# Optimization experiments

Measured on AMD Instinct MI355X. Metric: run time of the kernel, lower is better.

Reference implementation:

```python
import jax, jax.numpy as jnp
import numpy as np

B, S, C = 4, 4096, 1024
H, D, K = 16, 64, 256  # nhead, head_dim, dim_k


def setup_inputs() -> dict:
    key = jax.random.key(0)
    ks = jax.random.split(key, 7)
    x = jax.random.normal(ks[0], (B, S, C), dtype=jnp.float32)
    # per-head QKV projection weights (torch Linear weight layout [out,in])
    Wq = jax.random.normal(ks[1], (H, D, C), dtype=jnp.float32) * (C ** -0.5)
    Wk = jax.random.normal(ks[2], (H, D, C), dtype=jnp.float32) * (C ** -0.5)
    Wv = jax.random.normal(ks[3], (H, D, C), dtype=jnp.float32) * (C ** -0.5)
    # Linformer E/F sequence projections, per head: [K, S]
    We = jax.random.normal(ks[4], (H, K, S), dtype=jnp.float32) * (S ** -0.5)
    Wf = jax.random.normal(ks[5], (H, K, S), dtype=jnp.float32) * (S ** -0.5)
    # output projection (with bias, as w_o is nn.Linear default bias=True)
    Wo = jax.random.normal(ks[6], (C, H * D), dtype=jnp.float32) * ((H * D) ** -0.5)
    bo = jnp.zeros((C,), dtype=jnp.float32)
    return {"x": x, "Wq": Wq, "Wk": Wk, "Wv": Wv, "We": We, "Wf": Wf, "Wo": Wo, "bo": bo}


def reference(x, Wq, Wk, Wv, We, Wf, Wo, bo):
    # per-head projections: [B,H,S,D]
    Q = jnp.einsum('bsc,hdc->bhsd', x, Wq)
    Kh = jnp.einsum('bsc,hdc->bhsd', x, Wk)
    Vh = jnp.einsum('bsc,hdc->bhsd', x, Wv)
    # E-projection of K over the sequence axis: K^T [B,H,D,S] -> [B,H,D,K]
    Kp = jnp.einsum('bhsd,hks->bhdk', Kh, We)
    # scores: Q @ E(K^T) / sqrt(head_dim), softmax over low-rank axis k
    scale = 1.0 / jnp.sqrt(jnp.asarray(D, dtype=x.dtype))
    P = jax.nn.softmax(jnp.einsum('bhsd,bhdk->bhsk', Q, Kp) * scale, axis=-1)
    # F-projection of V over the sequence axis, then transpose back: [B,H,K,D]
    Vp = jnp.einsum('bhsd,hks->bhkd', Vh, Wf)
    out = jnp.einsum('bhsk,bhkd->bhsd', P, Vp)          # [B,H,S,D]
    out = out.transpose(0, 2, 1, 3).reshape(B, S, H * D)  # concat heads
    return jnp.einsum('bse,ce->bsc', out, Wo) + bo       # w_o (dropout=0)
```

## Files before the change

kernel.cpp:

```cpp
#include <hip/hip_runtime.h>
#include <stdint.h>


typedef unsigned short u16;
typedef __bf16 bf16t;
typedef bf16t bf16x8 __attribute__((ext_vector_type(8)));
typedef float f32x4 __attribute__((ext_vector_type(4)));

#define MFMA16(a, b, c) __builtin_amdgcn_mfma_f32_16x16x32_bf16((a), (b), (c), 0, 0, 0)

__device__ __forceinline__ u16 f2bf(float f) {
  return __builtin_bit_cast(u16, (bf16t)f);
}

__device__ __forceinline__ bf16x8 ldf(const u16* p) { return *(const bf16x8*)p; }

__device__ __forceinline__ void gload16(const void* g, void* l) {
  __builtin_amdgcn_global_load_lds(
      (__attribute__((address_space(1))) void*)g,
      (__attribute__((address_space(3))) void*)l, 16, 0, 0);
}

__device__ __forceinline__ int xcd_swz(int orig, int nwg) {
  return (orig & 7) * (nwg >> 3) + (orig >> 3);
}

__device__ __forceinline__ void gemm256_main(const u16* __restrict__ A,
                                             const u16* __restrict__ BT,
                                             int m0, int n0, f32x4 acc[8][4],
                                             u16* sm) {
  const int tid = threadIdx.x;
  const int w = tid >> 6, l = tid & 63, g = l >> 4, r = l & 15;
  const int wr = w >> 2, wc = w & 3;
  const int rowt = tid >> 3;
  const int cbsw = ((tid & 7) * 16) ^ ((rowt & 7) << 4);
  const int sxor = (r & 7) << 4;
  const char* Ab = (const char*)A;
  const char* Bb = (const char*)BT;
  char* smc = (char*)sm;

  auto stage = [&](int T, int buf) {
    const int k0 = T * 64;
#pragma unroll
    for (int i = 0; i < 4; ++i) {
      const int row = i * 64 + rowt;
      gload16(Ab + (((size_t)(m0 + row) << 10) + k0) * 2 + cbsw,
              smc + buf * 32768 + i * 8192 + w * 1024);
      gload16(Bb + (((size_t)(n0 + row) << 10) + k0) * 2 + cbsw,
              smc + 65536 + buf * 32768 + i * 8192 + w * 1024);
    }
  };

  stage(0, 0);
  for (int t = 0; t < 16; ++t) {
    const int b = t & 1;
    stage(t < 15 ? t + 1 : 15, b ^ 1);
    asm volatile("s_waitcnt vmcnt(8)" ::: "memory");
    __builtin_amdgcn_s_barrier();
    asm volatile("" ::: "memory");
    const char* At = smc + b * 32768;
    const char* Bt = smc + 65536 + b * 32768;
#pragma unroll
    for (int kk = 0; kk < 2; ++kk) {
      const int cb = (kk * 64 + g * 16) ^ sxor;
      bf16x8 af[8], bf[4];
#pragma unroll
      for (int m = 0; m < 8; ++m)
        af[m] = *(const bf16x8*)(At + ((wr * 128 + m * 16 + r) * 128 + cb));
#pragma unroll
      for (int n = 0; n < 4; ++n)
        bf[n] = *(const bf16x8*)(Bt + ((wc * 64 + n * 16 + r) * 128 + cb));
      __builtin_amdgcn_s_setprio(1);
#pragma unroll
      for (int m = 0; m < 8; ++m)
#pragma unroll
        for (int n = 0; n < 4; ++n)
          acc[m][n] = MFMA16(af[m], bf[n], acc[m][n]);
      __builtin_amdgcn_s_setprio(0);
    }
    asm volatile("" ::: "memory");
    __builtin_amdgcn_s_barrier();
    asm volatile("" ::: "memory");
  }
}

__global__ __launch_bounds__(256) void cvt_all(
    const float* __restrict__ x, const float* __restrict__ We,
    const float* __restrict__ Wf, const float* __restrict__ Wq,
    const float* __restrict__ Wk, const float* __restrict__ Wv,
    const float* __restrict__ Wo, u16* __restrict__ xb, u16* __restrict__ web,
    u16* __restrict__ wfb, u16* __restrict__ wqkv, u16* __restrict__ wob) {
  const int stride = gridDim.x * 256;
  for (int i = blockIdx.x * 256 + threadIdx.x; i < 13631488; i += stride) {
    const float4* s;
    ushort4* d;
    int off;
    if (i < 8388608) {
      if (i < 4194304) { s = (const float4*)x;  d = (ushort4*)xb;  off = i; }
      else             { s = (const float4*)We; d = (ushort4*)web; off = i - 4194304; }
    } else if (i < 12582912) { s = (const float4*)Wf; d = (ushort4*)wfb; off = i - 8388608; }
    else if (i < 12845056)   { s = (const float4*)Wq; d = (ushort4*)wqkv; off = i - 12582912; }
    else if (i < 13107200)   { s = (const float4*)Wk; d = (ushort4*)wqkv + 262144; off = i - 12845056; }
    else if (i < 13369344)   { s = (const float4*)Wv; d = (ushort4*)wqkv + 524288; off = i - 13107200; }
    else                     { s = (const float4*)Wo; d = (ushort4*)wob; off = i - 13369344; }
    float4 v = s[off];
    ushort4 o;
    o.x = f2bf(v.x); o.y = f2bf(v.y); o.z = f2bf(v.z); o.w = f2bf(v.w);
    d[off] = o;
  }
}

__global__ __launch_bounds__(512, 2) void gemm_q(const u16* __restrict__ A,
                                                 const u16* __restrict__ BT,
                                                 u16* __restrict__ Qd) {
  __shared__ u16 sm[65536];
  const int wg = xcd_swz(blockIdx.x, 256);
  const int m0 = (wg >> 2) * 256, n0 = (wg & 3) * 256;
  const int tid = threadIdx.x, w = tid >> 6, l = tid & 63, g = l >> 4, r = l & 15;
  const int wr = w >> 2, wc = w & 3;
  f32x4 acc[8][4] = {};
  gemm256_main(A, BT, m0, n0, acc, sm);
#pragma unroll
  for (int m = 0; m < 8; ++m)
#pragma unroll
    for (int n = 0; n < 4; ++n)
#pragma unroll
      for (int j = 0; j < 4; ++j) {
        const int mm = m0 + wr * 128 + m * 16 + g * 4 + j;
        const int nn = n0 + wc * 64 + n * 16 + r;
        const int b = mm >> 12, s = mm & 4095, h = nn >> 6, d = nn & 63;
        Qd[(((size_t)(b * 16 + h)) * 4096 + s) * 64 + d] = f2bf(acc[m][n][j] * 0.125f);
      }
}

__global__ __launch_bounds__(512, 2) void gemm_kv(const u16* __restrict__ A,
                                                  const u16* __restrict__ BT,
                                                  u16* __restrict__ KTd,
                                                  u16* __restrict__ VTd) {
  __shared__ u16 sm[65536];
  const int wg = xcd_swz(blockIdx.x, 512);
  const int m0 = (wg & 7) * 256, n0 = (wg >> 3) * 256;
  const int tid = threadIdx.x, w = tid >> 6, l = tid & 63, g = l >> 4, r = l & 15;
  const int wr = w >> 2, wc = w & 3;
  f32x4 acc[8][4] = {};
  gemm256_main(A, BT, m0, n0, acc, sm);
#pragma unroll
  for (int m = 0; m < 8; ++m)
#pragma unroll
    for (int n = 0; n < 4; ++n)
#pragma unroll
      for (int j = 0; j < 4; ++j) {
        const int mm = m0 + wr * 128 + m * 16 + g * 4 + j;
        const int nn = n0 + wc * 64 + n * 16 + r;
        const int which = mm >> 10, hd = mm & 1023, h = hd >> 6, d = hd & 63;
        const int b = nn >> 12, s = nn & 4095;
        u16* dst = which ? VTd : KTd;
        dst[(((size_t)(b * 16 + h)) * 64 + d) * 4096 + s] = f2bf(acc[m][n][j]);
      }
}

__global__ __launch_bounds__(512, 2) void gemm_out(const u16* __restrict__ A,
                                                   const u16* __restrict__ BT,
                                                   const float* __restrict__ bo,
                                                   float* __restrict__ out) {
  __shared__ u16 sm[65536];
  const int wg = xcd_swz(blockIdx.x, 256);
  const int m0 = (wg >> 2) * 256, n0 = (wg & 3) * 256;
  const int tid = threadIdx.x, w = tid >> 6, l = tid & 63, g = l >> 4, r = l & 15;
  const int wr = w >> 2, wc = w & 3;
  f32x4 acc[8][4] = {};
  gemm256_main(A, BT, m0, n0, acc, sm);
#pragma unroll
  for (int m = 0; m < 8; ++m)
#pragma unroll
    for (int n = 0; n < 4; ++n)
#pragma unroll
      for (int j = 0; j < 4; ++j) {
        const int mm = m0 + wr * 128 + m * 16 + g * 4 + j;
        const int nn = n0 + wc * 64 + n * 16 + r;
        out[(size_t)mm * 1024 + nn] = acc[m][n][j] + bo[nn];
      }
}

__global__ __launch_bounds__(256) void gemm_small(const u16* __restrict__ web,
                                                  const u16* __restrict__ wfb,
                                                  const u16* __restrict__ KT,
                                                  const u16* __restrict__ VT,
                                                  float* __restrict__ part) {
  __shared__ u16 ldsBig[256 * 64];
  __shared__ u16 ldsSml[64 * 64];
  const int bx = blockIdx.x, chunk = blockIdx.y;
  const int mode = bx & 1;
  const int bh = bx >> 1;
  const int hh = bh & 15;
  const u16 *Ap, *Bp;
  int M, N;
  u16 *ldsA, *ldsB;
  if (mode == 0) {
    Ap = web + (size_t)hh * 256 * 4096;
    Bp = KT + (size_t)bh * 64 * 4096;
    M = 256; N = 64;
    ldsA = ldsBig; ldsB = ldsSml;
  } else {
    Ap = VT + (size_t)bh * 64 * 4096;
    Bp = wfb + (size_t)hh * 256 * 4096;
    M = 64; N = 256;
    ldsA = ldsSml; ldsB = ldsBig;
  }
  float* Cpf = part + ((size_t)(mode * 4 + chunk) * 64 + bh) * 16384;
  const int tid = threadIdx.x, w = tid >> 6, l = tid & 63, g = l >> 4, r = l & 15;
  const int mb = (mode == 0) ? w * 64 : 0;
  const int nb = (mode == 0) ? 0 : w * 64;
  const int iA = (M * 8) / 256, iB = (N * 8) / 256;
  f32x4 acc[4][4] = {};
  for (int kt = chunk * 16; kt < chunk * 16 + 16; ++kt) {
    const int k0 = kt * 64;
    __syncthreads();
    for (int i = 0; i < iA; ++i) {
      const int c = w * (M * 2) + i * 64 + l;
      const int row = c >> 3, co = (c & 7) * 8;
      gload16(Ap + (size_t)row * 4096 + k0 + co, ldsA + (w * (M * 2) + i * 64) * 8);
    }
    for (int i = 0; i < iB; ++i) {
      const int c = w * (N * 2) + i * 64 + l;
      const int row = c >> 3, co = (c & 7) * 8;
      gload16(Bp + (size_t)row * 4096 + k0 + co, ldsB + (w * (N * 2) + i * 64) * 8);
    }
    __syncthreads();
#pragma unroll
    for (int kk = 0; kk < 2; ++kk) {
      bf16x8 af[4], bfv[4];
#pragma unroll
      for (int fm = 0; fm < 4; ++fm)
        af[fm] = ldf(ldsA + (mb + fm * 16 + r) * 64 + kk * 32 + g * 8);
#pragma unroll
      for (int fn = 0; fn < 4; ++fn)
        bfv[fn] = ldf(ldsB + (nb + fn * 16 + r) * 64 + kk * 32 + g * 8);
#pragma unroll
      for (int fm = 0; fm < 4; ++fm)
#pragma unroll
        for (int fn = 0; fn < 4; ++fn)
          acc[fm][fn] = MFMA16(af[fm], bfv[fn], acc[fm][fn]);
    }
  }
#pragma unroll
  for (int fm = 0; fm < 4; ++fm)
#pragma unroll
    for (int fn = 0; fn < 4; ++fn)
#pragma unroll
      for (int j = 0; j < 4; ++j) {
        const int m = mb + fm * 16 + g * 4 + j;
        const int n = nb + fn * 16 + r;
        Cpf[(size_t)m * N + n] = acc[fm][fn][j];
      }
}

__global__ __launch_bounds__(256) void reduce_small(const float* __restrict__ part,
                                                    u16* __restrict__ Kp,
                                                    u16* __restrict__ VpT) {
  const int i4 = blockIdx.x * 256 + threadIdx.x;
  const int mode = i4 >> 18;
  const int r4 = i4 & 262143;
  const float4* b = (const float4*)part;
  float4 s0 = b[(size_t)(mode * 4 + 0) * 262144 + r4];
  float4 s1 = b[(size_t)(mode * 4 + 1) * 262144 + r4];
  float4 s2 = b[(size_t)(mode * 4 + 2) * 262144 + r4];
  float4 s3 = b[(size_t)(mode * 4 + 3) * 262144 + r4];
  ushort4 o;
  o.x = f2bf(s0.x + s1.x + s2.x + s3.x);
  o.y = f2bf(s0.y + s1.y + s2.y + s3.y);
  o.z = f2bf(s0.z + s1.z + s2.z + s3.z);
  o.w = f2bf(s0.w + s1.w + s2.w + s3.w);
  ushort4* dst = (ushort4*)(mode ? VpT : Kp);
  dst[r4] = o;
}

__global__ __launch_bounds__(256, 1) void attn_fused(const u16* __restrict__ Q,
                                                     const u16* __restrict__ Kp,
                                                     const u16* __restrict__ VpT,
                                                     u16* __restrict__ att) {
  __shared__ u16 P[4][16 * 264];
  const int gid = blockIdx.x;
  const int bh = gid >> 3;
  const int st = gid & 7;
  const int hh = bh & 15, b = bh >> 4;
  const int tid = threadIdx.x, w = tid >> 6, l = tid & 63, g = l >> 4, r = l & 15;
  const u16* Kpb = Kp + (size_t)bh * 256 * 64;
  const u16* Vb = VpT + (size_t)bh * 64 * 256;

  bf16x8 kf[32];
  bf16x8 vf[32];
#pragma unroll
  for (int fn = 0; fn < 16; ++fn) {
    kf[fn * 2 + 0] = ldf(Kpb + (fn * 16 + r) * 64 + g * 8);
    kf[fn * 2 + 1] = ldf(Kpb + (fn * 16 + r) * 64 + 32 + g * 8);
  }
#pragma unroll
  for (int fn2 = 0; fn2 < 4; ++fn2)
#pragma unroll
    for (int kk = 0; kk < 8; ++kk)
      vf[fn2 * 8 + kk] = ldf(Vb + (fn2 * 16 + r) * 256 + kk * 32 + g * 8);

  u16* Pw = P[w];
  for (int t = 0; t < 8; ++t) {
    const int s0 = st * 512 + t * 64 + w * 16;
    const u16* Qb = Q + ((size_t)bh * 4096 + s0) * 64;
    const bf16x8 qf0 = ldf(Qb + r * 64 + g * 8);
    const bf16x8 qf1 = ldf(Qb + r * 64 + 32 + g * 8);
    f32x4 sc[16];
#pragma unroll
    for (int fn = 0; fn < 16; ++fn) {
      sc[fn] = MFMA16(qf0, kf[fn * 2 + 0], (f32x4){});
      sc[fn] = MFMA16(qf1, kf[fn * 2 + 1], sc[fn]);
    }
    float rinv[4];
#pragma unroll
    for (int j = 0; j < 4; ++j) {
      float sum = 0.f;
#pragma unroll
      for (int fn = 0; fn < 16; ++fn) {
        const float e = __expf(sc[fn][j]);
        sc[fn][j] = e;
        sum += e;
      }
      sum += __shfl_xor(sum, 1);
      sum += __shfl_xor(sum, 2);
      sum += __shfl_xor(sum, 4);
      sum += __shfl_xor(sum, 8);
      rinv[j] = 1.0f / sum;
    }
#pragma unroll
    for (int fn = 0; fn < 16; ++fn)
#pragma unroll
      for (int j = 0; j < 4; ++j)
        Pw[(g * 4 + j) * 264 + fn * 16 + r] = f2bf(sc[fn][j]);

    f32x4 o[4] = {};
#pragma unroll
    for (int kk = 0; kk < 8; ++kk) {
      const bf16x8 pa = ldf(Pw + r * 264 + kk * 32 + g * 8);
#pragma unroll
      for (int fn2 = 0; fn2 < 4; ++fn2)
        o[fn2] = MFMA16(pa, vf[fn2 * 8 + kk], o[fn2]);
    }
#pragma unroll
    for (int fn2 = 0; fn2 < 4; ++fn2)
#pragma unroll
      for (int j = 0; j < 4; ++j) {
        const int s = s0 + g * 4 + j;
        const int d = fn2 * 16 + r;
        att[((size_t)b * 4096 + s) * 1024 + hh * 64 + d] = f2bf(o[fn2][j] * rinv[j]);
      }
  }
}

extern "C" void kernel_launch(void* const* d_in, const int* in_sizes, int n_in,
                              void* d_out, int out_size, void* d_ws, size_t ws_size,
                              hipStream_t stream) {
  (void)in_sizes; (void)n_in; (void)out_size; (void)ws_size;
  const float* x  = (const float*)d_in[0];
  const float* Wq = (const float*)d_in[1];
  const float* Wk = (const float*)d_in[2];
  const float* Wv = (const float*)d_in[3];
  const float* We = (const float*)d_in[4];
  const float* Wf = (const float*)d_in[5];
  const float* Wo = (const float*)d_in[6];
  const float* bo = (const float*)d_in[7];
  char* ws = (char*)d_ws;
  u16* xb    = (u16*)(ws + 0);
  float* prt = (float*)(ws + 0);
  u16* att   = (u16*)(ws + 0);
  u16* wqkv  = (u16*)(ws + 33554432);
  u16* web   = (u16*)(ws + 39845888);
  u16* wfb   = (u16*)(ws + 73400320);
  u16* wob   = (u16*)(ws + 106954752);
  u16* Qd    = (u16*)(ws + 109051904);
  u16* KTd   = (u16*)(ws + 142606336);
  u16* VTd   = (u16*)(ws + 176160768);
  u16* Kpd   = (u16*)(ws + 209715200);
  u16* VpTd  = (u16*)(ws + 211812352);

  cvt_all<<<2048, 256, 0, stream>>>(x, We, Wf, Wq, Wk, Wv, Wo, xb, web, wfb, wqkv, wob);
  gemm_q<<<256, 512, 0, stream>>>(xb, wqkv, Qd);
  gemm_kv<<<512, 512, 0, stream>>>(wqkv + 1048576, xb, KTd, VTd);
  gemm_small<<<dim3(128, 4), 256, 0, stream>>>(web, wfb, KTd, VTd, prt);
  reduce_small<<<2048, 256, 0, stream>>>(prt, Kpd, VpTd);
  attn_fused<<<512, 256, 0, stream>>>(Qd, Kpd, VpTd, att);
  gemm_out<<<256, 512, 0, stream>>>(att, wob, bo, (float*)d_out);
}
```

Measured before the change: 328.1 us.

## Fuse We/Wf bf16 conversion into gemm_small loads with swizzled fp32 LDS

Removes the separate fp32→bf16 conversion pass over the large We and Wf sequence-projection weights. gemm_small now loads them as fp32 directly into XOR-swizzled LDS and converts to bf16 in registers just before the MFMAs. The remaining conversion is split into a vectorized 8-wide x converter and a small weight converter. This removes a full write and re-read of two 64 MB-class bf16 copies, at the cost of doubled LDS footprint, more global bytes read inside gemm_small (reused across batches), and extra conversion instructions in the inner loop.

```diff
diff --git a/kernel.cpp b/kernel.cpp
--- a/kernel.cpp
+++ b/kernel.cpp
@@ -6,6 +6,7 @@
 typedef __bf16 bf16t;
 typedef bf16t bf16x8 __attribute__((ext_vector_type(8)));
 typedef float f32x4 __attribute__((ext_vector_type(4)));
+typedef u16 u16x8 __attribute__((ext_vector_type(8)));
 
 #define MFMA16(a, b, c) __builtin_amdgcn_mfma_f32_16x16x32_bf16((a), (b), (c), 0, 0, 0)
 
@@ -84,30 +85,38 @@
   }
 }
 
-__global__ __launch_bounds__(256) void cvt_all(
-    const float* __restrict__ x, const float* __restrict__ We,
-    const float* __restrict__ Wf, const float* __restrict__ Wq,
-    const float* __restrict__ Wk, const float* __restrict__ Wv,
-    const float* __restrict__ Wo, u16* __restrict__ xb, u16* __restrict__ web,
-    u16* __restrict__ wfb, u16* __restrict__ wqkv, u16* __restrict__ wob) {
-  const int stride = gridDim.x * 256;
-  for (int i = blockIdx.x * 256 + threadIdx.x; i < 13631488; i += stride) {
-    const float4* s;
-    ushort4* d;
-    int off;
-    if (i < 8388608) {
-      if (i < 4194304) { s = (const float4*)x;  d = (ushort4*)xb;  off = i; }
-      else             { s = (const float4*)We; d = (ushort4*)web; off = i - 4194304; }
-    } else if (i < 12582912) { s = (const float4*)Wf; d = (ushort4*)wfb; off = i - 8388608; }
-    else if (i < 12845056)   { s = (const float4*)Wq; d = (ushort4*)wqkv; off = i - 12582912; }
-    else if (i < 13107200)   { s = (const float4*)Wk; d = (ushort4*)wqkv + 262144; off = i - 12845056; }
-    else if (i < 13369344)   { s = (const float4*)Wv; d = (ushort4*)wqkv + 524288; off = i - 13107200; }
-    else                     { s = (const float4*)Wo; d = (ushort4*)wob; off = i - 13369344; }
-    float4 v = s[off];
-    ushort4 o;
-    o.x = f2bf(v.x); o.y = f2bf(v.y); o.z = f2bf(v.z); o.w = f2bf(v.w);
-    d[off] = o;
-  }
+__global__ __launch_bounds__(256) void cvt_x(const float* __restrict__ src,
+                                             u16* __restrict__ dst) {
+  const size_t i = ((size_t)blockIdx.x * 256 + threadIdx.x) * 8;
+  const float4 a = *(const float4*)(src + i);
+  const float4 b = *(const float4*)(src + i + 4);
+  u16x8 o;
+  o[0] = f2bf(a.x); o[1] = f2bf(a.y); o[2] = f2bf(a.z); o[3] = f2bf(a.w);
+  o[4] = f2bf(b.x); o[5] = f2bf(b.y); o[6] = f2bf(b.z); o[7] = f2bf(b.w);
+  *(u16x8*)(dst + i) = o;
+}
+
+__global__ __launch_bounds__(256) void cvt_w(const float* __restrict__ Wq,
+                                             const float* __restrict__ Wk,
+                                             const float* __restrict__ Wv,
+                                             const float* __restrict__ Wo,
+                                             u16* __restrict__ wqkv,
+                                             u16* __restrict__ wob) {
+  const float* s;
+  u16* d;
+  switch (blockIdx.y) {
+    case 0: s = Wq; d = wqkv; break;
+    case 1: s = Wk; d = wqkv + 1048576; break;
+    case 2: s = Wv; d = wqkv + 2097152; break;
+    default: s = Wo; d = wob; break;
+  }
+  const size_t i = ((size_t)blockIdx.x * 256 + threadIdx.x) * 8;
+  const float4 a = *(const float4*)(s + i);
+  const float4 b = *(const float4*)(s + i + 4);
+  u16x8 o;
+  o[0] = f2bf(a.x); o[1] = f2bf(a.y); o[2] = f2bf(a.z); o[3] = f2bf(a.w);
+  o[4] = f2bf(b.x); o[5] = f2bf(b.y); o[6] = f2bf(b.z); o[7] = f2bf(b.w);
+  *(u16x8*)(d + i) = o;
 }
 
 __global__ __launch_bounds__(512, 2) void gemm_q(const u16* __restrict__ A,
@@ -182,77 +191,94 @@
       }
 }
 
-__global__ __launch_bounds__(256) void gemm_small(const u16* __restrict__ web,
-                                                  const u16* __restrict__ wfb,
+__global__ __launch_bounds__(256) void gemm_small(const float* __restrict__ WeF,
+                                                  const float* __restrict__ WfF,
                                                   const u16* __restrict__ KT,
                                                   const u16* __restrict__ VT,
                                                   float* __restrict__ part) {
-  __shared__ u16 ldsBig[256 * 64];
-  __shared__ u16 ldsSml[64 * 64];
+  __shared__ float ldsW[256 * 64];
+  __shared__ u16 ldsS[64 * 64];
   const int bx = blockIdx.x, chunk = blockIdx.y;
   const int mode = bx & 1;
   const int bh = bx >> 1;
   const int hh = bh & 15;
-  const u16 *Ap, *Bp;
-  int M, N;
-  u16 *ldsA, *ldsB;
-  if (mode == 0) {
-    Ap = web + (size_t)hh * 256 * 4096;
-    Bp = KT + (size_t)bh * 64 * 4096;
-    M = 256; N = 64;
-    ldsA = ldsBig; ldsB = ldsSml;
-  } else {
-    Ap = VT + (size_t)bh * 64 * 4096;
-    Bp = wfb + (size_t)hh * 256 * 4096;
-    M = 64; N = 256;
-    ldsA = ldsSml; ldsB = ldsBig;
-  }
+  const float* Wp = (mode == 0 ? WeF : WfF) + (size_t)hh * 256 * 4096;
+  const u16* Sp = (mode == 0 ? KT : VT) + (size_t)bh * 64 * 4096;
   float* Cpf = part + ((size_t)(mode * 4 + chunk) * 64 + bh) * 16384;
   const int tid = threadIdx.x, w = tid >> 6, l = tid & 63, g = l >> 4, r = l & 15;
-  const int mb = (mode == 0) ? w * 64 : 0;
-  const int nb = (mode == 0) ? 0 : w * 64;
-  const int iA = (M * 8) / 256, iB = (N * 8) / 256;
+  char* ldsWb = (char*)ldsW;
+  char* ldsSb = (char*)ldsS;
+  const int wcs = (tid & 15) ^ ((tid >> 4) & 7);
+  const int scs = (tid & 7) ^ ((tid >> 3) & 7);
   f32x4 acc[4][4] = {};
   for (int kt = chunk * 16; kt < chunk * 16 + 16; ++kt) {
     const int k0 = kt * 64;
     __syncthreads();
-    for (int i = 0; i < iA; ++i) {
-      const int c = w * (M * 2) + i * 64 + l;
-      const int row = c >> 3, co = (c & 7) * 8;
-      gload16(Ap + (size_t)row * 4096 + k0 + co, ldsA + (w * (M * 2) + i * 64) * 8);
-    }
-    for (int i = 0; i < iB; ++i) {
-      const int c = w * (N * 2) + i * 64 + l;
-      const int row = c >> 3, co = (c & 7) * 8;
-      gload16(Bp + (size_t)row * 4096 + k0 + co, ldsB + (w * (N * 2) + i * 64) * 8);
-    }
+#pragma unroll
+    for (int i = 0; i < 16; ++i)
+      gload16(Wp + (size_t)(i * 16 + (tid >> 4)) * 4096 + k0 + wcs * 4,
+              ldsWb + i * 4096 + w * 1024);
+#pragma unroll
+    for (int j = 0; j < 2; ++j)
+      gload16(Sp + (size_t)(j * 32 + (tid >> 3)) * 4096 + k0 + scs * 8,
+              ldsSb + j * 4096 + w * 1024);
     __syncthreads();
+    const int m8 = r & 7;
 #pragma unroll
     for (int kk = 0; kk < 2; ++kk) {
-      bf16x8 af[4], bfv[4];
-#pragma unroll
-      for (int fm = 0; fm < 4; ++fm)
-        af[fm] = ldf(ldsA + (mb + fm * 16 + r) * 64 + kk * 32 + g * 8);
+      bf16x8 wf8[4], sf8[4];
+#pragma unroll
+      for (int f = 0; f < 4; ++f) {
+        const int wrow = w * 64 + f * 16 + r;
+        const int c0 = (kk * 8 + g * 2) ^ m8;
+        const int c1 = (kk * 8 + g * 2 + 1) ^ m8;
+        const f32x4 lo = *(const f32x4*)(ldsWb + wrow * 256 + c0 * 16);
+        const f32x4 hi = *(const f32x4*)(ldsWb + wrow * 256 + c1 * 16);
+        bf16x8 o;
+#pragma unroll
+        for (int q = 0; q < 4; ++q) {
+          o[q] = (bf16t)lo[q];
+          o[q + 4] = (bf16t)hi[q];
+        }
+        wf8[f] = o;
+        const int srow = f * 16 + r;
+        const int sc = (kk * 4 + g) ^ m8;
+        sf8[f] = *(const bf16x8*)(ldsSb + srow * 128 + sc * 16);
+      }
+      if (mode == 0) {
+#pragma unroll
+        for (int fm = 0; fm < 4; ++fm)
+#pragma unroll
+          for (int fn = 0; fn < 4; ++fn)
+            acc[fm][fn] = MFMA16(wf8[fm], sf8[fn], acc[fm][fn]);
+      } else {
+#pragma unroll
+        for (int fm = 0; fm < 4; ++fm)
+#pragma unroll
+          for (int fn = 0; fn < 4; ++fn)
+            acc[fm][fn] = MFMA16(sf8[fm], wf8[fn], acc[fm][fn]);
+      }
+    }
+  }
+  if (mode == 0) {
+#pragma unroll
+    for (int fm = 0; fm < 4; ++fm)
 #pragma unroll
       for (int fn = 0; fn < 4; ++fn)
-        bfv[fn] = ldf(ldsB + (nb + fn * 16 + r) * 64 + kk * 32 + g * 8);
-#pragma unroll
-      for (int fm = 0; fm < 4; ++fm)
-#pragma unroll
-        for (int fn = 0; fn < 4; ++fn)
-          acc[fm][fn] = MFMA16(af[fm], bfv[fn], acc[fm][fn]);
-    }
-  }
-#pragma unroll
-  for (int fm = 0; fm < 4; ++fm)
-#pragma unroll
-    for (int fn = 0; fn < 4; ++fn)
-#pragma unroll
-      for (int j = 0; j < 4; ++j) {
-        const int m = mb + fm * 16 + g * 4 + j;
-        const int n = nb + fn * 16 + r;
-        Cpf[(size_t)m * N + n] = acc[fm][fn][j];
-      }
+#pragma unroll
+        for (int j = 0; j < 4; ++j)
+          Cpf[(size_t)(w * 64 + fm * 16 + g * 4 + j) * 64 + fn * 16 + r] =
+              acc[fm][fn][j];
+  } else {
+#pragma unroll
+    for (int fm = 0; fm < 4; ++fm)
+#pragma unroll
+      for (int fn = 0; fn < 4; ++fn)
+#pragma unroll
+        for (int j = 0; j < 4; ++j)
+          Cpf[(size_t)(fm * 16 + g * 4 + j) * 256 + w * 64 + fn * 16 + r] =
+              acc[fm][fn][j];
+  }
 }
 
 __global__ __launch_bounds__(256) void reduce_small(const float* __restrict__ part,
@@ -371,8 +397,6 @@
   float* prt = (float*)(ws + 0);
   u16* att   = (u16*)(ws + 0);
   u16* wqkv  = (u16*)(ws + 33554432);
-  u16* web   = (u16*)(ws + 39845888);
-  u16* wfb   = (u16*)(ws + 73400320);
   u16* wob   = (u16*)(ws + 106954752);
   u16* Qd    = (u16*)(ws + 109051904);
   u16* KTd   = (u16*)(ws + 142606336);
@@ -380,10 +404,11 @@
   u16* Kpd   = (u16*)(ws + 209715200);
   u16* VpTd  = (u16*)(ws + 211812352);
 
-  cvt_all<<<2048, 256, 0, stream>>>(x, We, Wf, Wq, Wk, Wv, Wo, xb, web, wfb, wqkv, wob);
+  cvt_x<<<8192, 256, 0, stream>>>(x, xb);
+  cvt_w<<<dim3(512, 4), 256, 0, stream>>>(Wq, Wk, Wv, Wo, wqkv, wob);
   gemm_q<<<256, 512, 0, stream>>>(xb, wqkv, Qd);
   gemm_kv<<<512, 512, 0, stream>>>(wqkv + 1048576, xb, KTd, VTd);
-  gemm_small<<<dim3(128, 4), 256, 0, stream>>>(web, wfb, KTd, VTd, prt);
+  gemm_small<<<dim3(128, 4), 256, 0, stream>>>(We, Wf, KTd, VTd, prt);
   reduce_small<<<2048, 256, 0, stream>>>(prt, Kpd, VpTd);
   attn_fused<<<512, 256, 0, stream>>>(Qd, Kpd, VpTd, att);
   gemm_out<<<256, 512, 0, stream>>>(att, wob, bo, (float*)d_out);
```

New measurement: 315.8 us. -3.7%, faster.
